# Kernel optimization log

Hardware: AMD Instinct MI355X
Metric: run time of the kernel (lower is better)

Reference implementation:

```python
import jax, jax.numpy as jnp
import numpy as np

B, S, N, E = 8, 64, 512, 32  # batch, seq_size, node_num, embed_size


def setup_inputs() -> dict:
    key = jax.random.key(0)
    k0, k1, k2, k3, k4 = jax.random.split(key, 5)
    x = jax.random.normal(k0, (B, S, N), dtype=jnp.float32)
    # lin_w: Linear(2*S, E) -> weight (E, 2*S), bias (E,)
    W = jax.random.normal(k1, (E, 2 * S), dtype=jnp.float32) * (1.0 / np.sqrt(2 * S))
    b_w = jax.random.normal(k2, (E,), dtype=jnp.float32) * 0.01
    # lin_a: Linear(E, 1) -> weight (E,), bias scalar
    Wa = jax.random.normal(k3, (E,), dtype=jnp.float32) * (1.0 / np.sqrt(E))
    b_a = jax.random.normal(k4, (), dtype=jnp.float32) * 0.01
    return {"x": x, "W": W, "b_w": b_w, "Wa": Wa, "b_a": b_a}


def reference(x, W, b_w, Wa, b_a):
    # Faithful to MP_GAT.forward in eval mode (dropout = identity).
    # Algebraic decomposition: lin_w(cat(vi, vj)) = vi @ Wi^T + vj @ Wj^T + b,
    # where W = [Wi | Wj] along the input dim -- avoids the O(N^2 * 2S) concat.
    s = W.shape[1] // 2
    v = jnp.transpose(x, (0, 2, 1))          # (B, N, S)
    Wi, Wj = W[:, :s], W[:, s:]              # (E, S) each
    ti = jnp.einsum('bns,es->bne', v, Wi)    # (B, N, E)
    tj = jnp.einsum('bns,es->bne', v, Wj)    # (B, N, E)
    pre = ti[:, :, None, :] + tj[:, None, :, :] + b_w  # (B, N, N, E)
    xw = jnp.where(pre > 0, pre, 0.2 * pre)  # LeakyReLU(0.2)
    e = jnp.einsum('bije,e->bij', xw, Wa) + b_a        # (B, N, N) = lin_a(...).squeeze
    attention = jax.nn.softmax(e, axis=2)
    h = jax.nn.sigmoid(jnp.einsum('bij,bjs->bis', attention, v))  # (B, N, S)
    return jnp.transpose(h, (0, 2, 1)), attention      # (B, S, N), (B, N, N)
```

## Files before the change

kernel.cpp:

```cpp
#include <hip/hip_runtime.h>
#include <math.h>

#define BB 8
#define SS 64
#define NN 512
#define EE 32
#define IT 8

typedef __attribute__((ext_vector_type(8))) short short8v;
typedef __attribute__((ext_vector_type(4))) float f32x4;

__device__ __forceinline__ unsigned short f2bf(float f) {
    union { float f; unsigned u; } v; v.f = f;
    unsigned r = v.u + 0x7fffu + ((v.u >> 16) & 1u);
    return (unsigned short)(r >> 16);
}
__device__ __forceinline__ float bflo(unsigned u) { return __uint_as_float(u << 16); }
__device__ __forceinline__ float bfhi(unsigned u) { return __uint_as_float(u & 0xffff0000u); }
__device__ __forceinline__ unsigned packtr(float lo, float hi) {
    return (__float_as_uint(hi) & 0xffff0000u) | (__float_as_uint(lo) >> 16);
}

__global__ __launch_bounds__(128) void proj_kernel(
    const float* __restrict__ x, const float* __restrict__ W,
    const float* __restrict__ b_w, const float* __restrict__ Wa,
    float* __restrict__ tip, unsigned short* __restrict__ tjb,
    float* __restrict__ cip, float* __restrict__ djp)
{
    __shared__ float sW[SS][65];
    const int t = threadIdx.x;
    const int wg = ((blockIdx.x & 7) << 6) | (blockIdx.x >> 3);
    const int b = wg >> 6;
    const int n0 = (wg & 63) << 3;

#pragma unroll
    for (int r = 0; r < 8; ++r) {
        int idx = r * 512 + t * 4;
        float4 w4 = *(const float4*)(W + idx);
        int e = idx >> 7;
        int sp = idx & 127;
        int eo = ((sp >> 6) << 5) | e;
        int s0 = sp & 63;
        sW[s0 + 0][eo] = w4.x;
        sW[s0 + 1][eo] = w4.y;
        sW[s0 + 2][eo] = w4.z;
        sW[s0 + 3][eo] = w4.w;
    }
    __syncthreads();

    const int eo = t & 63;
    const int ng = t >> 6;
    const float* xb = x + (size_t)b * SS * NN + n0 + (ng << 2);
    float a0 = 0.f, a1 = 0.f, a2 = 0.f, a3 = 0.f;
#pragma unroll 8
    for (int s = 0; s < SS; ++s) {
        float wv = sW[s][eo];
        float4 xv = *(const float4*)(xb + (size_t)s * NN);
        a0 = fmaf(wv, xv.x, a0);
        a1 = fmaf(wv, xv.y, a1);
        a2 = fmaf(wv, xv.z, a2);
        a3 = fmaf(wv, xv.w, a3);
    }
    const int e = eo & 31;
    const bool isI = eo < EE;
    if (isI) {
        float bias = b_w[e];
        a0 += bias; a1 += bias; a2 += bias; a3 += bias;
        *(float4*)(tip + ((size_t)(b * EE + e)) * NN + n0 + (ng << 2)) =
            make_float4(a0, a1, a2, a3);
    } else {
        unsigned u0 = f2bf(a0) | ((unsigned)f2bf(a1) << 16);
        unsigned u1 = f2bf(a2) | ((unsigned)f2bf(a3) << 16);
        *(uint2*)(tjb + ((size_t)(b * EE + e)) * NN + n0 + (ng << 2)) =
            make_uint2(u0, u1);
    }

    float wa = Wa[e];
    float r0 = wa * a0, r1 = wa * a1, r2 = wa * a2, r3 = wa * a3;
#pragma unroll
    for (int off = 1; off <= 16; off <<= 1) {
        r0 += __shfl_xor(r0, off);
        r1 += __shfl_xor(r1, off);
        r2 += __shfl_xor(r2, off);
        r3 += __shfl_xor(r3, off);
    }
    if (eo == 0)
        *(float4*)(cip + (size_t)b * NN + n0 + (ng << 2)) = make_float4(r0, r1, r2, r3);
    if (eo == 32)
        *(float4*)(djp + (size_t)b * NN + n0 + (ng << 2)) = make_float4(r0, r1, r2, r3);
}

__global__ __launch_bounds__(512, 2) void attn_kernel(
    const float* __restrict__ x,
    const float* __restrict__ tip,
    const unsigned short* __restrict__ tjb,
    const float* __restrict__ cip,
    const float* __restrict__ djp,
    const float* __restrict__ Wa,
    float* __restrict__ out0,
    float* __restrict__ out1)
{
    __shared__ __align__(16) unsigned short stj[EE * NN];
    __shared__ __align__(16) unsigned short prT[IT * 520];
    __shared__ __align__(16) float s_tiT[IT][36];
    __shared__ __align__(16) float hp[2][SS][12];
    __shared__ __align__(16) float red[8][IT];
    __shared__ float s_inv[IT];

    const int t = threadIdx.x;
    const int wg = ((blockIdx.x & 7) << 6) | (blockIdx.x >> 3);
    const int b = wg >> 6;
    const int i0 = (wg & 63) << 3;
    const int lane = t & 63;
    const int w = t >> 6;

    if (t < 256) {
        int i = t & 7, e = t >> 3;
        s_tiT[i][e] = tip[((size_t)(b * EE + e)) * NN + i0 + i];
    }
    {
        const uint4* src = (const uint4*)(tjb + (size_t)b * EE * NN);
        uint4* dst = (uint4*)stj;
#pragma unroll
        for (int r = 0; r < 4; ++r) dst[r * 512 + t] = src[r * 512 + t];
    }
    __syncthreads();

    const int ip = t & 3;
    const int j0 = t & ~3;
    const int ia = 2 * ip, ib2 = 2 * ip + 1;

    float rti0[EE], rti1[EE];
#pragma unroll
    for (int q = 0; q < 8; ++q) {
        float4 v = *(const float4*)&s_tiT[ia][q << 2];
        rti0[4 * q + 0] = v.x; rti0[4 * q + 1] = v.y;
        rti0[4 * q + 2] = v.z; rti0[4 * q + 3] = v.w;
        float4 u = *(const float4*)&s_tiT[ib2][q << 2];
        rti1[4 * q + 0] = u.x; rti1[4 * q + 1] = u.y;
        rti1[4 * q + 2] = u.z; rti1[4 * q + 3] = u.w;
    }

    float acc0[4], acc1[4];
#pragma unroll
    for (int k = 0; k < 4; ++k) { acc0[k] = 0.f; acc1[k] = 0.f; }

#pragma unroll
    for (int e = 0; e < EE; ++e) {
        uint2 d = *(const uint2*)&stj[e * NN + j0];
        float wa = Wa[e];
        float t0 = rti0[e], t1 = rti1[e];
        float tjf[4];
        tjf[0] = bflo(d.x); tjf[1] = bfhi(d.x);
        tjf[2] = bflo(d.y); tjf[3] = bfhi(d.y);
#pragma unroll
        for (int k = 0; k < 4; ++k) {
            acc0[k] = fmaf(fabsf(t0 + tjf[k]), wa, acc0[k]);
            acc1[k] = fmaf(fabsf(t1 + tjf[k]), wa, acc1[k]);
        }
    }

    float4 dj4 = *(const float4*)(djp + (size_t)b * NN + j0);
    float dj[4] = {dj4.x, dj4.y, dj4.z, dj4.w};
    float c0 = cip[(size_t)b * NN + i0 + ia];
    float c1 = cip[(size_t)b * NN + i0 + ib2];
    float pr0[4], pr1[4];
#pragma unroll
    for (int k = 0; k < 4; ++k) {
        pr0[k] = __expf(fmaf(0.4f, acc0[k], 0.6f * (c0 + dj[k])));
        pr1[k] = __expf(fmaf(0.4f, acc1[k], 0.6f * (c1 + dj[k])));
    }

    {
        uint2 pa, pb;
        pa.x = f2bf(pr0[0]) | ((unsigned)f2bf(pr0[1]) << 16);
        pa.y = f2bf(pr0[2]) | ((unsigned)f2bf(pr0[3]) << 16);
        pb.x = f2bf(pr1[0]) | ((unsigned)f2bf(pr1[1]) << 16);
        pb.y = f2bf(pr1[2]) | ((unsigned)f2bf(pr1[3]) << 16);
        *(uint2*)&prT[ia * 520 + j0]  = pa;
        *(uint2*)&prT[ib2 * 520 + j0] = pb;
    }

    float rs0 = pr0[0] + pr0[1] + pr0[2] + pr0[3];
    float rs1 = pr1[0] + pr1[1] + pr1[2] + pr1[3];
#pragma unroll
    for (int off = 4; off <= 32; off <<= 1) {
        rs0 += __shfl_xor(rs0, off);
        rs1 += __shfl_xor(rs1, off);
    }
    if (lane < 4) { red[w][2 * lane] = rs0; red[w][2 * lane + 1] = rs1; }
    __syncthreads();
    if (t < IT) {
        float S = 0.f;
#pragma unroll
        for (int ww = 0; ww < 8; ++ww) S += red[ww][t];
        s_inv[t] = 1.0f / S;
    }
    __syncthreads();

    {
        float v0 = s_inv[ia], v1 = s_inv[ib2];
        *(float4*)(out1 + ((size_t)(b * NN + i0 + ia)) * NN + j0) =
            make_float4(pr0[0]*v0, pr0[1]*v0, pr0[2]*v0, pr0[3]*v0);
        *(float4*)(out1 + ((size_t)(b * NN + i0 + ib2)) * NN + j0) =
            make_float4(pr1[0]*v1, pr1[1]*v1, pr1[2]*v1, pr1[3]*v1);
    }

    {
        const int mt = w & 3;
        const int kh = w >> 2;
        const int lm = lane & 15;
        const int ko = lane >> 4;
        const float* xrow = x + ((size_t)(b * SS + mt * 16 + lm)) * NN;

        f32x4 acc = {0.f, 0.f, 0.f, 0.f};
#pragma unroll
        for (int st = 0; st < 8; ++st) {
            const int j = kh * 256 + st * 32 + ko * 8;
            float4 xa = *(const float4*)(xrow + j);
            float4 xb2 = *(const float4*)(xrow + j + 4);
            union { unsigned u[4]; short8v v; } af;
            af.u[0] = packtr(xa.x, xa.y);
            af.u[1] = packtr(xa.z, xa.w);
            af.u[2] = packtr(xb2.x, xb2.y);
            af.u[3] = packtr(xb2.z, xb2.w);
            short8v bf = *(const short8v*)&prT[(lm & 7) * 520 + j];
            acc = __builtin_amdgcn_mfma_f32_16x16x32_bf16(af.v, bf, acc, 0, 0, 0);
        }
        if (lm < 8) {
#pragma unroll
            for (int r = 0; r < 4; ++r) {
                int s = mt * 16 + (lane >> 4) * 4 + r;
                hp[kh][s][lm] = acc[r];
            }
        }
    }
    __syncthreads();

    {
        int i = t & 7, s = t >> 3;
        float h = (hp[0][s][i] + hp[1][s][i]) * s_inv[i];
        out0[((size_t)(b * SS + s)) * NN + i0 + i] = 1.0f / (1.0f + __expf(-h));
    }
}

extern "C" void kernel_launch(void* const* d_in, const int* in_sizes, int n_in,
                              void* d_out, int out_size, void* d_ws, size_t ws_size,
                              hipStream_t stream) {
    const float* x   = (const float*)d_in[0];
    const float* W   = (const float*)d_in[1];
    const float* b_w = (const float*)d_in[2];
    const float* Wa  = (const float*)d_in[3];

    float* out0 = (float*)d_out;
    float* out1 = (float*)d_out + (size_t)BB * SS * NN;

    float* tip = (float*)d_ws;
    unsigned short* tjb = (unsigned short*)(tip + (size_t)BB * EE * NN);
    float* cip = (float*)(tjb + (size_t)BB * EE * NN);
    float* djp = cip + (size_t)BB * NN;

    proj_kernel<<<BB * (NN / 8), 128, 0, stream>>>(x, W, b_w, Wa, tip, tjb, cip, djp);
    attn_kernel<<<BB * (NN / IT), 512, 0, stream>>>(x, tip, tjb, cip, djp, Wa, out0, out1);
}
```

Measured before the change: 23.14 us.

## Process 16 query rows per 1024-thread block and remap softmax reduction

Doubles the rows handled per workgroup to 16 with 1024 threads. Each thread now covers a contiguous j-chunk for two rows, so row sums reduce within a wave and a 2-wave pair, and one barrier plus the s_inv stage disappear. The staged tj tile is now reused across 16 rows instead of 8, and the MFMA uses all 16 columns rather than 8 with a 4-way K split. The trade-off is half as many blocks (256), a single-block occupancy bound, and higher register pressure per thread.

```diff
diff --git a/kernel.cpp b/kernel.cpp
--- a/kernel.cpp
+++ b/kernel.cpp
@@ -5,7 +5,7 @@
 #define SS 64
 #define NN 512
 #define EE 32
-#define IT 8
+#define IT 16
 
 typedef __attribute__((ext_vector_type(8))) short short8v;
 typedef __attribute__((ext_vector_type(4))) float f32x4;
@@ -90,7 +90,7 @@
         *(float4*)(djp + (size_t)b * NN + n0 + (ng << 2)) = make_float4(r0, r1, r2, r3);
 }
 
-__global__ __launch_bounds__(512, 2) void attn_kernel(
+__global__ __launch_bounds__(1024, 1) void attn_kernel(
     const float* __restrict__ x,
     const float* __restrict__ tip,
     const unsigned short* __restrict__ tjb,
@@ -103,31 +103,31 @@
     __shared__ __align__(16) unsigned short stj[EE * NN];
     __shared__ __align__(16) unsigned short prT[IT * 520];
     __shared__ __align__(16) float s_tiT[IT][36];
-    __shared__ __align__(16) float hp[2][SS][12];
-    __shared__ __align__(16) float red[8][IT];
-    __shared__ float s_inv[IT];
+    __shared__ __align__(16) float hp[4][SS][17];
+    __shared__ __align__(16) float red[16][2];
 
     const int t = threadIdx.x;
-    const int wg = ((blockIdx.x & 7) << 6) | (blockIdx.x >> 3);
-    const int b = wg >> 6;
-    const int i0 = (wg & 63) << 3;
+    const int wg = ((blockIdx.x & 7) << 5) | (blockIdx.x >> 3);
+    const int b = wg >> 5;
+    const int i0 = (wg & 31) << 4;
     const int lane = t & 63;
     const int w = t >> 6;
 
-    if (t < 256) {
-        int i = t & 7, e = t >> 3;
+    if (t < 512) {
+        int i = t & 15, e = t >> 4;
         s_tiT[i][e] = tip[((size_t)(b * EE + e)) * NN + i0 + i];
     }
     {
         const uint4* src = (const uint4*)(tjb + (size_t)b * EE * NN);
         uint4* dst = (uint4*)stj;
 #pragma unroll
-        for (int r = 0; r < 4; ++r) dst[r * 512 + t] = src[r * 512 + t];
-    }
-    __syncthreads();
-
-    const int ip = t & 3;
-    const int j0 = t & ~3;
+        for (int r = 0; r < 2; ++r) dst[r * 1024 + t] = src[r * 1024 + t];
+    }
+    __syncthreads();
+
+    const int ip = t >> 7;
+    const int jc = t & 127;
+    const int j0 = jc << 2;
     const int ia = 2 * ip, ib2 = 2 * ip + 1;
 
     float rti0[EE], rti1[EE];
@@ -184,39 +184,32 @@
     float rs0 = pr0[0] + pr0[1] + pr0[2] + pr0[3];
     float rs1 = pr1[0] + pr1[1] + pr1[2] + pr1[3];
 #pragma unroll
-    for (int off = 4; off <= 32; off <<= 1) {
+    for (int off = 1; off <= 32; off <<= 1) {
         rs0 += __shfl_xor(rs0, off);
         rs1 += __shfl_xor(rs1, off);
     }
-    if (lane < 4) { red[w][2 * lane] = rs0; red[w][2 * lane + 1] = rs1; }
-    __syncthreads();
-    if (t < IT) {
-        float S = 0.f;
-#pragma unroll
-        for (int ww = 0; ww < 8; ++ww) S += red[ww][t];
-        s_inv[t] = 1.0f / S;
-    }
-    __syncthreads();
-
-    {
-        float v0 = s_inv[ia], v1 = s_inv[ib2];
-        *(float4*)(out1 + ((size_t)(b * NN + i0 + ia)) * NN + j0) =
-            make_float4(pr0[0]*v0, pr0[1]*v0, pr0[2]*v0, pr0[3]*v0);
-        *(float4*)(out1 + ((size_t)(b * NN + i0 + ib2)) * NN + j0) =
-            make_float4(pr1[0]*v1, pr1[1]*v1, pr1[2]*v1, pr1[3]*v1);
-    }
+    if (lane == 0) { red[w][0] = rs0; red[w][1] = rs1; }
+    __syncthreads();
+
+    float inv0 = 1.0f / (red[2 * ip][0] + red[2 * ip + 1][0]);
+    float inv1 = 1.0f / (red[2 * ip][1] + red[2 * ip + 1][1]);
+
+    *(float4*)(out1 + ((size_t)(b * NN + i0 + ia)) * NN + j0) =
+        make_float4(pr0[0]*inv0, pr0[1]*inv0, pr0[2]*inv0, pr0[3]*inv0);
+    *(float4*)(out1 + ((size_t)(b * NN + i0 + ib2)) * NN + j0) =
+        make_float4(pr1[0]*inv1, pr1[1]*inv1, pr1[2]*inv1, pr1[3]*inv1);
 
     {
         const int mt = w & 3;
-        const int kh = w >> 2;
+        const int kq = w >> 2;
         const int lm = lane & 15;
         const int ko = lane >> 4;
         const float* xrow = x + ((size_t)(b * SS + mt * 16 + lm)) * NN;
 
         f32x4 acc = {0.f, 0.f, 0.f, 0.f};
 #pragma unroll
-        for (int st = 0; st < 8; ++st) {
-            const int j = kh * 256 + st * 32 + ko * 8;
+        for (int st = 0; st < 4; ++st) {
+            const int j = kq * 128 + st * 32 + ko * 8;
             float4 xa = *(const float4*)(xrow + j);
             float4 xb2 = *(const float4*)(xrow + j + 4);
             union { unsigned u[4]; short8v v; } af;
@@ -224,22 +217,21 @@
             af.u[1] = packtr(xa.z, xa.w);
             af.u[2] = packtr(xb2.x, xb2.y);
             af.u[3] = packtr(xb2.z, xb2.w);
-            short8v bf = *(const short8v*)&prT[(lm & 7) * 520 + j];
+            short8v bf = *(const short8v*)&prT[lm * 520 + j];
             acc = __builtin_amdgcn_mfma_f32_16x16x32_bf16(af.v, bf, acc, 0, 0, 0);
         }
-        if (lm < 8) {
-#pragma unroll
-            for (int r = 0; r < 4; ++r) {
-                int s = mt * 16 + (lane >> 4) * 4 + r;
-                hp[kh][s][lm] = acc[r];
-            }
+#pragma unroll
+        for (int r = 0; r < 4; ++r) {
+            int s = mt * 16 + (lane >> 4) * 4 + r;
+            hp[kq][s][lm] = acc[r];
         }
     }
     __syncthreads();
 
     {
-        int i = t & 7, s = t >> 3;
-        float h = (hp[0][s][i] + hp[1][s][i]) * s_inv[i];
+        int i = t & 15, s = t >> 4;
+        float inv = 1.0f / (red[2 * (i >> 1)][i & 1] + red[2 * (i >> 1) + 1][i & 1]);
+        float h = ((hp[0][s][i] + hp[1][s][i]) + (hp[2][s][i] + hp[3][s][i])) * inv;
         out0[((size_t)(b * SS + s)) * NN + i0 + i] = 1.0f / (1.0f + __expf(-h));
     }
 }
@@ -261,5 +253,5 @@
     float* djp = cip + (size_t)BB * NN;
 
     proj_kernel<<<BB * (NN / 8), 128, 0, stream>>>(x, W, b_w, Wa, tip, tjb, cip, djp);
-    attn_kernel<<<BB * (NN / IT), 512, 0, stream>>>(x, tip, tjb, cip, djp, Wa, out0, out1);
-}
+    attn_kernel<<<BB * (NN / IT), 1024, 0, stream>>>(x, tip, tjb, cip, djp, Wa, out0, out1);
+}
```

After: 20.52 us. 11.3% less time.
